# Performance work log

Hardware: AMD Instinct MI355X
Metric: run time of the kernel (lower is better)

Reference implementation:

```python
import jax, jax.numpy as jnp
import numpy as np

N_USERS = 20000
N_ITEMS = 30000
N = N_USERS + N_ITEMS          # total nodes
D = 64                          # embedding_dim
EXTRA = 1152                    # 768 metadata + 384 review
E = 500000                      # full-graph edges
NC = 100                        # clusters
HEADS = 2                       # per-layer GATConv heads
CG_HEADS = 4                    # GlobalGATOverClusters hard-codes heads=4
L = 2                           # num_layers
ED = 2                          # edge_dim


def _gat(x, ei, ea, lin, a_src, a_dst, lin_e, a_edge, bias, heads, nnodes):
    """PyG GATConv: add self loops (edge_attr fill='mean'), concat=False -> head mean."""
    C = a_src.shape[-1]
    loop = jnp.arange(nnodes)
    src = jnp.concatenate([ei[0], loop])
    dst = jnp.concatenate([ei[1], loop])
    ea_full = jnp.concatenate([ea, jnp.broadcast_to(ea.mean(0), (nnodes, ea.shape[1]))], 0)
    xh = (x @ lin).reshape(nnodes, heads, C)            # [N,H,C]
    asrc = (xh * a_src).sum(-1)                         # [N,H]
    adst = (xh * a_dst).sum(-1)
    eh = (ea_full @ lin_e).reshape(-1, heads, C)        # [Etot,H,C]
    ae = (eh * a_edge).sum(-1)                          # [Etot,H]
    al = jax.nn.leaky_relu(asrc[src] + adst[dst] + ae, 0.2)
    amax = jax.ops.segment_max(al, dst, num_segments=nnodes)
    ex = jnp.exp(al - amax[dst])
    s = jax.ops.segment_sum(ex, dst, num_segments=nnodes)
    w = ex / (s[dst] + 1e-16)
    out = jax.ops.segment_sum(xh[src] * w[..., None], dst, num_segments=nnodes)
    return out.mean(1) + bias


def _graph_norm(x, weight, bias, mean_scale, eps=1e-5):
    mean = x.mean(0)
    out = x - mean_scale * mean
    var = (out * out).mean(0)
    return weight * out * jax.lax.rsqrt(var + eps) + bias


def _forward(product_extra_features, user_emb, item_emb, fus_w1, fus_b1, fus_w2, fus_b2,
             full_edge_attr, gcn_w, gcn_b,
             cg_lin, cg_att_src, cg_att_dst, cg_lin_edge, cg_att_edge, cg_bias, cluster_edge_attr,
             gat_lin, gat_att_src, gat_att_dst, gat_lin_edge, gat_att_edge, gat_bias,
             gn_weight, gn_bias, gn_mean_scale,
             full_edge_index, cluster_assignment, cluster_edge_index):
    # fusion MLP on item side (dropout is identity at inference)
    h = jnp.maximum(jnp.concatenate([item_emb, product_extra_features], -1) @ fus_w1 + fus_b1, 0.0)
    enriched_items = h @ fus_w2 + fus_b2
    X = jnp.concatenate([user_emb, enriched_items], 0)  # [N, D]

    # per-cluster GCN == one GCN over intra-cluster edges + self loops;
    # nodes in clusters with zero intra edges keep original features
    ei0, ei1 = full_edge_index[0], full_edge_index[1]
    intra = cluster_assignment[ei0] == cluster_assignment[ei1]
    loop = jnp.arange(N)
    row = jnp.concatenate([ei0, loop])
    col = jnp.concatenate([ei1, loop])
    ew = jnp.concatenate([intra.astype(X.dtype), jnp.ones((N,), X.dtype)])
    deg = jax.ops.segment_sum(ew, col, num_segments=N)
    dinv = jnp.where(deg > 0, jax.lax.rsqrt(deg), 0.0)
    norm = dinv[row] * ew * dinv[col]
    xw = X @ gcn_w
    gcn_out = jax.ops.segment_sum(xw[row] * norm[:, None], col, num_segments=N) + gcn_b
    cl_has_edge = jax.ops.segment_sum(intra.astype(jnp.int32), cluster_assignment[ei0], num_segments=NC) > 0
    Xc = jnp.where(cl_has_edge[cluster_assignment][:, None], gcn_out, X)

    # mean pool per cluster
    cnt = jax.ops.segment_sum(jnp.ones((N,), X.dtype), cluster_assignment, num_segments=NC)
    pooled = jax.ops.segment_sum(Xc, cluster_assignment, num_segments=NC) / jnp.maximum(cnt, 1.0)[:, None]

    # global GAT over clusters (inter-cluster multigraph, precomputed)
    cl_upd = _gat(pooled, cluster_edge_index, cluster_edge_attr,
                  cg_lin, cg_att_src, cg_att_dst, cg_lin_edge, cg_att_edge, cg_bias, CG_HEADS, NC)
    Xcomb = Xc + cl_upd[cluster_assignment]

    # full-graph GAT stack with GraphNorm + residual ELU (dropout identity)
    for i in range(L):
        Xin = Xcomb
        g = _gat(Xcomb, full_edge_index, full_edge_attr,
                 gat_lin[i], gat_att_src[i], gat_att_dst[i],
                 gat_lin_edge[i], gat_att_edge[i], gat_bias[i], HEADS, N)
        g = _graph_norm(g, gn_weight[i], gn_bias[i], gn_mean_scale[i])
        Xcomb = jax.nn.elu(g + Xin)

    return Xcomb[:N_USERS], Xcomb[N_USERS:]


def setup_inputs() -> dict:
    rng = np.random.default_rng(0)
    fei = rng.integers(0, N, size=(2, E)).astype(np.int32)
    ca = rng.integers(0, NC, size=(N,)).astype(np.int32)
    fea = rng.random((E, ED)).astype(np.float32)
    # build_cluster_graph: one cluster edge per inter-cluster full edge
    cu, cv = ca[fei[0]], ca[fei[1]]
    m = cu != cv
    cei = np.stack([cu[m], cv[m]]).astype(np.int32)
    cea = fea[m]

    key = jax.random.key(0)
    ks = jax.random.split(key, 24)
    nrm = lambda k, shp, s=0.05: jax.random.normal(k, shp, dtype=jnp.float32) * s
    return {
        'product_extra_features': jax.random.normal(ks[0], (N_ITEMS, EXTRA), dtype=jnp.float32),
        'user_emb': nrm(ks[1], (N_USERS, D), 1.0),
        'item_emb': nrm(ks[2], (N_ITEMS, D), 1.0),
        'fus_w1': nrm(ks[3], (D + EXTRA, 2 * D)),
        'fus_b1': jnp.zeros((2 * D,), jnp.float32),
        'fus_w2': nrm(ks[4], (2 * D, D)),
        'fus_b2': jnp.zeros((D,), jnp.float32),
        'full_edge_attr': jnp.asarray(fea),
        'gcn_w': nrm(ks[5], (D, D)),
        'gcn_b': jnp.zeros((D,), jnp.float32),
        'cg_lin': nrm(ks[6], (D, CG_HEADS * D)),
        'cg_att_src': nrm(ks[7], (CG_HEADS, D)),
        'cg_att_dst': nrm(ks[8], (CG_HEADS, D)),
        'cg_lin_edge': nrm(ks[9], (ED, CG_HEADS * D)),
        'cg_att_edge': nrm(ks[10], (CG_HEADS, D)),
        'cg_bias': jnp.zeros((D,), jnp.float32),
        'cluster_edge_attr': jnp.asarray(cea),
        'gat_lin': nrm(ks[11], (L, D, HEADS * D)),
        'gat_att_src': nrm(ks[12], (L, HEADS, D)),
        'gat_att_dst': nrm(ks[13], (L, HEADS, D)),
        'gat_lin_edge': nrm(ks[14], (L, ED, HEADS * D)),
        'gat_att_edge': nrm(ks[15], (L, HEADS, D)),
        'gat_bias': jnp.zeros((L, D), jnp.float32),
        'gn_weight': jnp.ones((L, D), jnp.float32),
        'gn_bias': jnp.zeros((L, D), jnp.float32),
        'gn_mean_scale': jnp.ones((L, D), jnp.float32),
        'full_edge_index': jnp.asarray(fei),
        'cluster_assignment': jnp.asarray(ca),
        'cluster_edge_index': jnp.asarray(cei),
    }


def reference(product_extra_features, user_emb, item_emb, fus_w1, fus_b1, fus_w2, fus_b2,
              full_edge_attr, gcn_w, gcn_b,
              cg_lin, cg_att_src, cg_att_dst, cg_lin_edge, cg_att_edge, cg_bias, cluster_edge_attr,
              gat_lin, gat_att_src, gat_att_dst, gat_lin_edge, gat_att_edge, gat_bias,
              gn_weight, gn_bias, gn_mean_scale,
              full_edge_index, cluster_assignment, cluster_edge_index):
    return _forward(product_extra_features, user_emb, item_emb, fus_w1, fus_b1, fus_w2, fus_b2,
                    full_edge_attr, gcn_w, gcn_b,
                    cg_lin, cg_att_src, cg_att_dst, cg_lin_edge, cg_att_edge, cg_bias, cluster_edge_attr,
                    gat_lin, gat_att_src, gat_att_dst, gat_lin_edge, gat_att_edge, gat_bias,
                    gn_weight, gn_bias, gn_mean_scale,
                    full_edge_index, cluster_assignment, cluster_edge_index)
```

## Files before the change

kernel.cpp:

```cpp
#include <hip/hip_runtime.h>
#include <hip/hip_bf16.h>

#define N_USERS 20000
#define N_ITEMS 30000
#define NTOT    50000
#define DIM     64
#define EXTRA_D 1152
#define E_EDGES 500000
#define NC      100
#define KTOT    1216
#define KSTEPS  38
#define PPART   16
#define SPART   128

#define B_FEI  1954
#define B_W1   608
#define B_W2   32
#define B_CEI  256
#define PREP_GRID (B_FEI+B_W1+B_W2+B_CEI)

#define FUS_BLKS ((N_ITEMS+127)/128)
#define SCAN1_BLKS ((NTOT+1023)/1024)
#define B_COPY 1250
#define B_CC   64
#define FUS_GRID (FUS_BLKS+SCAN1_BLKS+1+B_COPY+B_CC)

#define SC3_BLKS ((NTOT+255)/256)
#define FILL_BLKS ((E_EDGES+255)/256)
#define DEG_BLKS ((NTOT+3)/4)

typedef __attribute__((ext_vector_type(8))) short short8;
typedef __attribute__((ext_vector_type(4))) float v4f;

__device__ __forceinline__ float wred_sum(float v){
#pragma unroll
  for(int o=32;o;o>>=1) v += __shfl_xor(v,o,64);
  return v;
}
__device__ __forceinline__ int wred_sumi(int v){
#pragma unroll
  for(int o=32;o;o>>=1) v += __shfl_xor(v,o,64);
  return v;
}
__device__ __forceinline__ float lrelu(float x){ return x>0.f? x : 0.2f*x; }
__device__ __forceinline__ short f2bf(float f){
  unsigned u=__float_as_uint(f);
  unsigned r=(u + 0x7FFFu + ((u>>16)&1u))>>16;
  return (short)r;
}
__device__ __forceinline__ unsigned pack_bf2(float x, float y){
  return (unsigned)(unsigned short)f2bf(x) | ((unsigned)(unsigned short)f2bf(y)<<16);
}

__global__ __launch_bounds__(256) void prep_edges_kernel(
    const float* __restrict__ w1, short* __restrict__ w1t,
    const float* __restrict__ w2, short* __restrict__ w2t,
    const int* __restrict__ ca,
    const int* __restrict__ fei, const float* __restrict__ fea,
    int* __restrict__ cnt_dst, int* __restrict__ clflag, int* __restrict__ degI,
    float2* __restrict__ partA,
    const int* __restrict__ cei, const float* __restrict__ cea, int Ec,
    int* __restrict__ ccnt_dst, float2* __restrict__ partB)
{
  __shared__ int hist[NC];
  __shared__ float2 w4[4];
  const int b=blockIdx.x, t=threadIdx.x;
  const int lane=t&63, wv=t>>6;
  if(b < B_FEI){
    int e = b*256+t;
    float a0=0.f,a1=0.f;
    if(e<E_EDGES){
      int s=fei[e], d=fei[E_EDGES+e];
      atomicAdd(&cnt_dst[d],1);
      int cs=ca[s];
      if(cs==ca[d]){ clflag[cs]=1; atomicAdd(&degI[d],1); }
      float2 v=*(const float2*)(fea+2*e);
      a0=v.x; a1=v.y;
    }
    a0=wred_sum(a0); a1=wred_sum(a1);
    if(lane==0) w4[wv]=make_float2(a0,a1);
    __syncthreads();
    if(t==0){ float2 r=w4[0]; for(int i=1;i<4;i++){r.x+=w4[i].x; r.y+=w4[i].y;} partA[b]=r; }
  } else if(b < B_FEI+B_W1){
    int i = (b-B_FEI)*256+t;
    int row = i>>7, n = i&127;
    int s = row>>5, kk = row&31;
    w1t[s*4096 + n*32 + kk] = f2bf(w1[i]);
  } else if(b < B_FEI+B_W1+B_W2){
    int i = (b-B_FEI-B_W1)*256+t;
    int n = i>>6, c = i&63;
    w2t[c*128 + n] = f2bf(w2[i]);
  } else {
    int bb = b-(B_FEI+B_W1+B_W2);
    for(int i=t;i<NC;i+=256) hist[i]=0;
    __syncthreads();
    float a0=0.f,a1=0.f;
    for(int e=bb*256+t; e<Ec; e+=B_CEI*256){
      atomicAdd(&hist[cei[Ec+e]],1);
      float2 v=*(const float2*)(cea+2*e);
      a0+=v.x; a1+=v.y;
    }
    a0=wred_sum(a0); a1=wred_sum(a1);
    if(lane==0) w4[wv]=make_float2(a0,a1);
    __syncthreads();
// ... 233 lines not shown
    for(int i=t;i<4096;i+=256) Wl[i]=gw[i];
    __syncthreads();
    for(int r=bb*4+wv; r<NTOT; r+=1024*4){
      rowb[wv][lane]=X[(size_t)r*64+lane];
      float acc=0.f;
#pragma unroll 8
      for(int k=0;k<64;k++) acc+=rowb[wv][k]*Wl[k*64+lane];
      xw[(size_t)r*64+lane]=acc;
    }
  }
}

__global__ __launch_bounds__(256) void fill_kernel(
    const int* __restrict__ fei, const float* __restrict__ fea,
    int* __restrict__ fillptr, int2* __restrict__ slot2,
    const int* __restrict__ cei, const float* __restrict__ cea, int Ec,
    int* __restrict__ cfillp, int* __restrict__ cslot_src, float2* __restrict__ cslot_ea)
{
  __shared__ int hist[NC];
  __shared__ int base[NC];
  const int b=blockIdx.x, t=threadIdx.x;
  if(b<FILL_BLKS){
    int e=b*256+t;
    if(e<E_EDGES){
      int dst=fei[E_EDGES+e], src=fei[e];
      int pos=atomicAdd(&fillptr[dst],1);
      float2 v=*(const float2*)(fea+2*e);
      slot2[pos]=make_int2(src,(int)pack_bf2(v.x,v.y));
    }
  } else {
    int bb=b-FILL_BLKS;
    const int chunk=(Ec+127)/128;
    const int beg=bb*chunk;
    const int end=min(beg+chunk,Ec);
    for(int i=t;i<NC;i+=256) hist[i]=0;
    __syncthreads();
    for(int e=beg+t;e<end;e+=256) atomicAdd(&hist[cei[Ec+e]],1);
    __syncthreads();
    for(int i=t;i<NC;i+=256){
      int h=hist[i];
      base[i] = h ? atomicAdd(&cfillp[i],h) : 0;
      hist[i]=0;
    }
    __syncthreads();
    for(int e=beg+t;e<end;e+=256){
      int d=cei[Ec+e];
      int pos = base[d] + atomicAdd(&hist[d],1);
      cslot_src[pos]=cei[e];
      cslot_ea[pos]=make_float2(cea[2*e],cea[2*e+1]);
    }
  }
}

__global__ __launch_bounds__(256) void gcn_agg_kernel(const float* __restrict__ X,
    const float* __restrict__ xw, const float* __restrict__ gcn_b,
    const int* __restrict__ offs, const int2* __restrict__ slot2, const int* __restrict__ ca,
    const float* __restrict__ dinv, const int* __restrict__ flag,
    float* __restrict__ Xc, float* __restrict__ psum){
  __shared__ float2 stg[4][64];
  int lane=threadIdx.x&63, wv=threadIdx.x>>6;
  int n=blockIdx.x*4+wv;
  int beg=offs[n], end=offs[n+1], myca=ca[n];
  float acc=0.f;
  for(int c0=beg;c0<end;c0+=64){
    int j=c0+lane;
    float coef=0.f; int s=0;
    if(j<end){
      s=slot2[j].x;
      if(ca[s]==myca) coef=dinv[s];
    }
    stg[wv][lane]=make_float2(__int_as_float(s),coef);
    unsigned long long bal=__ballot(coef!=0.f);
    while(bal){
      int k=__builtin_ctzll(bal); bal&=bal-1;
      float2 sc=stg[wv][k];
      acc += sc.y * xw[(size_t)__float_as_int(sc.x)*64+lane];
    }
  }
  float gout = dinv[n]*acc + gcn_b[lane];
  float xc = flag[myca] ? gout : X[(size_t)n*64+lane];
  Xc[(size_t)n*64+lane]=xc;
  atomicAdd(&psum[(size_t)(blockIdx.x&(PPART-1))*NC*64 + myca*64+lane], xc);
}

__global__ __launch_bounds__(256) void cluster_prep_kernel(const float* __restrict__ psum,
    const int* __restrict__ ccnt, const float* __restrict__ cg_lin,
    const float* __restrict__ as_, const float* __restrict__ ad_,
    float* __restrict__ xh_c, float* __restrict__ asrc_c, float* __restrict__ adst_c){
  __shared__ float prow[64];
  const int c=blockIdx.x, t=threadIdx.x;
  if(t<64){
    float a=0.f;
#pragma unroll
    for(int p=0;p<PPART;p++) a += psum[(size_t)p*NC*64 + c*64 + t];
    prow[t]=a/fmaxf((float)ccnt[c],1.f);
  }
  __syncthreads();
  float acc=0.f;
#pragma unroll 8
  for(int k=0;k<64;k++) acc += prow[k]*cg_lin[k*256+t];
  xh_c[c*256+t]=acc;
  int lane=t&63, hh=t>>6;
  float s=wred_sum(acc*as_[hh*64+lane]);
  float d=wred_sum(acc*ad_[hh*64+lane]);
  if(lane==0){ asrc_c[c*4+hh]=s; adst_c[c*4+hh]=d; }
}
__global__ __launch_bounds__(256) void cluster_agg_kernel(
    const int* __restrict__ coffs, const int* __restrict__ cslot_src, const float2* __restrict__ cslot_ea,
    const float* __restrict__ asrc_c, const float* __restrict__ adst_c, const float* __restrict__ coefs,
    const float* __restrict__ xh_c, const float* __restrict__ cg_bias, float* __restrict__ cl_upd)
{
  __shared__ float sas[NC*4];
  __shared__ float sW[NC*4];
  __shared__ float ssum[4];
  __shared__ float red[4][64];
  const int c=blockIdx.x, t=threadIdx.x;
  for(int i=t;i<NC*4;i+=256){ sas[i]=asrc_c[i]; sW[i]=0.f; }
  __syncthreads();
  float ad[4], A0[4], A1[4];
#pragma unroll
  for(int h=0;h<4;h++){ ad[h]=adst_c[c*4+h]; A0[h]=coefs[8+h]; A1[h]=coefs[12+h]; }
  const int beg=coffs[c], end=coffs[c+1];
  for(int j=beg+t;j<end;j+=256){
    int s=cslot_src[j]; float2 e=cslot_ea[j];
#pragma unroll
    for(int h=0;h<4;h++){
      float al=lrelu(sas[s*4+h]+ad[h]+e.x*A0[h]+e.y*A1[h]);
      atomicAdd(&sW[s*4+h], __expf(al));
    }
  }
  if(t<4){
    float al=lrelu(sas[c*4+t]+ad[t]+coefs[6]*A0[t]+coefs[7]*A1[t]);
    atomicAdd(&sW[c*4+t], __expf(al));
  }
  __syncthreads();
  const int h=t>>6, lane=t&63;
  float p=0.f;
  if(lane<NC)    p += sW[lane*4+h];
  if(lane+64<NC) p += sW[(lane+64)*4+h];
  p=wred_sum(p);
  if(lane==0) ssum[h]=p+1e-16f;
  __syncthreads();
  float inv=1.f/ssum[h];
  float acc=0.f;
  for(int s=0;s<NC;s++) acc += sW[s*4+h]*xh_c[s*256+h*64+lane];
  red[h][lane]=acc*inv;
  __syncthreads();
  if(t<64) cl_upd[c*64+t]=0.25f*(red[0][t]+red[1][t]+red[2][t]+red[3][t])+cg_bias[t];
}

__global__ __launch_bounds__(256) void gat_xh0_kernel(const float* __restrict__ Xc,
    const float* __restrict__ cl_upd, const int* __restrict__ ca,
    const float* __restrict__ lin, const float* __restrict__ att_s, const float* __restrict__ att_d,
    float2* __restrict__ xh2, float* __restrict__ asrc, float* __restrict__ adst,
    float* __restrict__ Xa){
  __shared__ __align__(16) float Wl[64*128];
  __shared__ float rowb[4][64];
  int t=threadIdx.x;
  for(int i=t;i<8192;i+=256) Wl[i]=lin[i];
  __syncthreads();
  int lane=t&63, wv=t>>6;
  float as0=att_s[lane], as1=att_s[64+lane], ad0=att_d[lane], ad1=att_d[64+lane];
  for(int r=blockIdx.x*4+wv; r<NTOT; r+=gridDim.x*4){
    float xv = Xc[(size_t)r*64+lane] + cl_upd[ca[r]*64+lane];
    Xa[(size_t)r*64+lane]=xv;
    rowb[wv][lane]=xv;
    float x0=0.f,x1=0.f;
#pragma unroll 8
    for(int k=0;k<64;k++){ float q=rowb[wv][k]; x0+=q*Wl[k*128+lane]; x1+=q*Wl[k*128+64+lane]; }
    xh2[(size_t)r*64+lane]=make_float2(x0,x1);
    float p0=wred_sum(x0*as0);
    float p1=wred_sum(x1*as1);
    float q0=wred_sum(x0*ad0);
    float q1=wred_sum(x1*ad1);
    if(lane==0){ asrc[2*r]=p0; asrc[2*r+1]=p1; adst[2*r]=q0; adst[2*r+1]=q1; }
  }
}
__global__ __launch_bounds__(256) void gat_xh1_kernel(const float* __restrict__ g,
    const float* __restrict__ Xres, const float* __restrict__ spart,
    const float* __restrict__ gnw, const float* __restrict__ gnb, const float* __restrict__ gnms,
    const float* __restrict__ lin, const float* __restrict__ att_s, const float* __restrict__ att_d,
    float2* __restrict__ xh2, float* __restrict__ asrc, float* __restrict__ adst,
    float* __restrict__ Xb){
  __shared__ __align__(16) float Wl[64*128];
  __shared__ float rowb[4][64];
  __shared__ float sm[4][64], sv[4][64];
  int t=threadIdx.x;
  int lane=t&63, wv=t>>6;
  for(int i=t;i<8192;i+=256) Wl[i]=lin[i];
  {
    float a0=0.f,a1=0.f;
    for(int p=wv;p<SPART;p+=4){ a0+=spart[p*128+lane]; a1+=spart[p*128+64+lane]; }
    sm[wv][lane]=a0; sv[wv][lane]=a1;
  }
  __syncthreads();
  const float invN = 1.f/(float)NTOT;
  float m=(sm[0][lane]+sm[1][lane]+sm[2][lane]+sm[3][lane])*invN;
  float vsum=(sv[0][lane]+sv[1][lane]+sv[2][lane]+sv[3][lane])*invN;
  float mm=gnms[lane]*m;
  float gwv=rsqrtf(vsum - 2.f*mm*m + mm*mm + 1e-5f)*gnw[lane];
  float gbv=gnb[lane];
  float as0=att_s[lane], as1=att_s[64+lane], ad0=att_d[lane], ad1=att_d[64+lane];
  for(int r=blockIdx.x*4+wv; r<NTOT; r+=gridDim.x*4){
    float z=(g[(size_t)r*64+lane]-mm)*gwv+gbv + Xres[(size_t)r*64+lane];
    float xv = z>0.f? z : __expf(z)-1.f;
    Xb[(size_t)r*64+lane]=xv;
    rowb[wv][lane]=xv;
    float x0=0.f,x1=0.f;
#pragma unroll 8
    for(int k=0;k<64;k++){ float q=rowb[wv][k]; x0+=q*Wl[k*128+lane]; x1+=q*Wl[k*128+64+lane]; }
    xh2[(size_t)r*64+lane]=make_float2(x0,x1);
    float p0=wred_sum(x0*as0);
    float p1=wred_sum(x1*as1);
    float q0=wred_sum(x0*ad0);
    float q1=wred_sum(x1*ad1);
    if(lane==0){ asrc[2*r]=p0; asrc[2*r+1]=p1; adst[2*r]=q0; adst[2*r+1]=q1; }
  }
}

__global__ __launch_bounds__(256) void gat_agg_kernel(const float2* __restrict__ xh2,
    const float2* __restrict__ asrc, const float2* __restrict__ adst,
    const int* __restrict__ offs, const int2* __restrict__ slot2,
    const float* __restrict__ coefs, int layer, const float* __restrict__ bias,
    float* __restrict__ g, float* __restrict__ spart){
  __shared__ float4 stg[4][64];
  __shared__ float s1[64], s2[64];
  int t=threadIdx.x;
  int lane=t&63, wv=t>>6;
  if(t<64){ s1[t]=0.f; s2[t]=0.f; }
  __syncthreads();
  int n=blockIdx.x*4+wv;
  float A00=coefs[16+layer*2+0], A01=coefs[16+layer*2+1];
  float A10=coefs[20+layer*2+0], A11=coefs[20+layer*2+1];
  int beg=offs[n], end=offs[n+1];
  float2 adn=adst[n];
  float s0=0.f,sB=0.f,acc0=0.f,acc1=0.f;
  for(int c0=beg;c0<end;c0+=64){
    int j=c0+lane;
    float ex0=0.f,ex1=0.f; int s=0;
    if(j<end){
      int2 sl=slot2[j];
      s=sl.x;
      unsigned p=(unsigned)sl.y;
      float e0=__uint_as_float(p<<16);
      float e1=__uint_as_float(p&0xffff0000u);
      float2 a=asrc[s];
      ex0=__expf(lrelu(a.x+adn.x+e0*A00+e1*A10));
      ex1=__expf(lrelu(a.y+adn.y+e0*A01+e1*A11));
    }
    s0+=ex0; sB+=ex1;
    stg[wv][lane]=make_float4(__int_as_float(s),ex0,ex1,0.f);
    int cnt=min(64,end-c0);
    int k=0;
    for(; k+4<=cnt; k+=4){
      float4 w0=stg[wv][k], w1=stg[wv][k+1], w2=stg[wv][k+2], w3=stg[wv][k+3];
      float2 x0=xh2[(size_t)__float_as_int(w0.x)*64+lane];
      float2 x1=xh2[(size_t)__float_as_int(w1.x)*64+lane];
      float2 x2=xh2[(size_t)__float_as_int(w2.x)*64+lane];
      float2 x3=xh2[(size_t)__float_as_int(w3.x)*64+lane];
      acc0 += w0.y*x0.x + w1.y*x1.x + w2.y*x2.x + w3.y*x3.x;
      acc1 += w0.z*x0.y + w1.z*x1.y + w2.z*x2.y + w3.z*x3.y;
    }
    for(; k<cnt; k++){
      float4 ws=stg[wv][k];
      float2 xv=xh2[(size_t)__float_as_int(ws.x)*64+lane];
      acc0 += ws.y*xv.x;
      acc1 += ws.z*xv.y;
    }
  }
  s0=wred_sum(s0); sB=wred_sum(sB);
  float gv = 0.5f*(acc0/(s0+1e-16f)+acc1/(sB+1e-16f))+bias[lane];
  g[(size_t)n*64+lane]=gv;
  atomicAdd(&s1[lane],gv);
  atomicAdd(&s2[lane],gv*gv);
  __syncthreads();
  float* dstp = spart + (size_t)(blockIdx.x&(SPART-1))*128;
  if(t<64) atomicAdd(&dstp[t],s1[t]);
  else if(t<128) atomicAdd(&dstp[t],s2[t-64]);
}

__global__ __launch_bounds__(256) void gnorm_elu_kernel(const float* __restrict__ g,
    const float* __restrict__ Xin, const float* __restrict__ spart,
    const float* __restrict__ gw, const float* __restrict__ gb, const float* __restrict__ gms,
    float* __restrict__ outp){
  __shared__ float sst[2][128];
  const float invN = 1.f/(float)NTOT;
  int t=threadIdx.x;
  {
    int d=t&127, hf=t>>7;
    float a=0.f;
    for(int p=hf*64;p<hf*64+64;p++) a+=spart[p*128+d];
    sst[hf][d]=a;
  }
  __syncthreads();
  int i0=blockIdx.x*256+t;
  int d0=(i0&15)*4;
  float mmv[4],gwv[4],gbv[4];
#pragma unroll
  for(int j=0;j<4;j++){
    int d=d0+j;
    float m=(sst[0][d]+sst[1][d])*invN;
    float mm=gms[d]*m;
    mmv[j]=mm;
    gwv[j]=rsqrtf((sst[0][64+d]+sst[1][64+d])*invN-2.f*mm*m+mm*mm+1e-5f)*gw[d];
    gbv[j]=gb[d];
  }
  for(int i=i0;i<NTOT*16;i+=gridDim.x*256){
    float4 gv=((const float4*)g)[i];
    float4 xv=((const float4*)Xin)[i];
    float4 o; float z;
    z=(gv.x-mmv[0])*gwv[0]+gbv[0]+xv.x; o.x = z>0.f? z : __expf(z)-1.f;
    z=(gv.y-mmv[1])*gwv[1]+gbv[1]+xv.y; o.y = z>0.f? z : __expf(z)-1.f;
    z=(gv.z-mmv[2])*gwv[2]+gbv[2]+xv.z; o.z = z>0.f? z : __expf(z)-1.f;
    z=(gv.w-mmv[3])*gwv[3]+gbv[3]+xv.w; o.w = z>0.f? z : __expf(z)-1.f;
    ((float4*)outp)[i]=o;
  }
}

extern "C" void kernel_launch(void* const* d_in, const int* in_sizes, int n_in,
                              void* d_out, int out_size, void* d_ws, size_t ws_size,
                              hipStream_t stream)
{
  const float* extra = (const float*)d_in[0];
  const float* user  = (const float*)d_in[1];
  const float* item  = (const float*)d_in[2];
  const float* fw1 = (const float*)d_in[3];
  const float* fb1 = (const float*)d_in[4];
  const float* fw2 = (const float*)d_in[5];
  const float* fb2 = (const float*)d_in[6];
  const float* fea = (const float*)d_in[7];
  const float* gcn_w = (const float*)d_in[8];
  const float* gcn_b = (const float*)d_in[9];
  const float* cg_lin = (const float*)d_in[10];
  const float* cg_as = (const float*)d_in[11];
  const float* cg_ad = (const float*)d_in[12];
  const float* cg_le = (const float*)d_in[13];
  const float* cg_ae = (const float*)d_in[14];
  const float* cg_bias = (const float*)d_in[15];
  const float* cea = (const float*)d_in[16];
  const float* gat_lin = (const float*)d_in[17];
  const float* gat_as = (const float*)d_in[18];
  const float* gat_ad = (const float*)d_in[19];
  const float* gat_le = (const float*)d_in[20];
  const float* gat_ae = (const float*)d_in[21];
  const float* gat_bias = (const float*)d_in[22];
  const float* gn_w = (const float*)d_in[23];
  const float* gn_b = (const float*)d_in[24];
  const float* gn_ms = (const float*)d_in[25];
  const int* fei = (const int*)d_in[26];
  const int* ca  = (const int*)d_in[27];
  const int* cei = (const int*)d_in[28];
  const int Ec = in_sizes[16]/2;
  float* outp = (float*)d_out;

  char* w = (char*)d_ws;
  auto alloc=[&](size_t b)->char*{ char* p=w; w += (b+255)&~(size_t)255; return p; };

  char* z0 = w;
  int* cnt_dst = (int*)alloc((size_t)NTOT*4);
  int* degI = (int*)alloc((size_t)NTOT*4);
  int* clflag = (int*)alloc(NC*4);
  int* ccnt = (int*)alloc(NC*4);
  int* ccnt_dst = (int*)alloc(NC*4);
  float* psum = (float*)alloc((size_t)PPART*NC*64*4);
  float* spart0 = (float*)alloc((size_t)SPART*128*4);
  float* spart1 = (float*)alloc((size_t)SPART*128*4);
  size_t zbytes = (size_t)(w - z0);

  float2* partA = (float2*)alloc(2048*8);
  float2* partB = (float2*)alloc(256*8);
  float* coefs = (float*)alloc(32*4);
  int* offs = (int*)alloc((size_t)(NTOT+1)*4);
  int* incl = (int*)alloc((size_t)NTOT*4);
  int* bsum = (int*)alloc(64*4);
  int* fillptr = (int*)alloc((size_t)NTOT*4);
  int2* slot2 = (int2*)alloc((size_t)(E_EDGES+NTOT)*8);
  int* coffs = (int*)alloc((size_t)(NC+1)*4);
  int* cfillp = (int*)alloc((size_t)NC*4);
  int* cslot_src = (int*)alloc((size_t)E_EDGES*4);
  float2* cslot_ea = (float2*)alloc((size_t)E_EDGES*8);
  float* dinv = (float*)alloc((size_t)NTOT*4);
  float* xh_c = (float*)alloc(NC*256*4);
  float* asrc_c = (float*)alloc(NC*4*4);
  float* adst_c = (float*)alloc(NC*4*4);
  float* cl_upd = (float*)alloc(NC*64*4);
  float* asrc = (float*)alloc((size_t)NTOT*2*4);
  float* adst = (float*)alloc((size_t)NTOT*2*4);
  short* w1t = (short*)alloc((size_t)KSTEPS*4096*2);
  short* w2t = (short*)alloc((size_t)64*128*2);
  float* bufA = (float*)alloc((size_t)NTOT*64*4);
  float* bufB = (float*)alloc((size_t)NTOT*64*4);
  float* bufC = (float*)alloc((size_t)NTOT*64*4);
  float* bufD = (float*)alloc((size_t)NTOT*64*4);
  float* bufE = (float*)alloc((size_t)NTOT*128*4);

  float* X  = bufA; float* g  = bufA;
  float* Xc = bufB;
  float* xw = bufC; float* Xb = bufC;
  float* Xa = bufD;
  float2* xh2 = (float2*)bufE;

  hipMemsetAsync(z0, 0, zbytes, stream);

  prep_edges_kernel<<<PREP_GRID,256,0,stream>>>(fw1, w1t, fw2, w2t, ca,
                                              fei, fea, cnt_dst, clflag, degI, partA,
                                              cei, cea, Ec, ccnt_dst, partB);
  fus_scan_kernel<<<FUS_GRID,256,0,stream>>>(item, extra, w1t, fb1, w2t, fb2, X,
                                              partA, partB, Ec, cg_le, cg_ae, gat_le, gat_ae, coefs,
                                              cnt_dst, incl, bsum, user, ca, ccnt);
  mid_kernel<<<SC3_BLKS+1+1024,256,0,stream>>>(incl, cnt_dst, bsum, offs, fillptr, coefs, slot2,
                                              degI, dinv, ccnt_dst, coffs, cfillp,
                                              X, gcn_w, xw);
  fill_kernel<<<FILL_BLKS+128,256,0,stream>>>(fei, fea, fillptr, slot2,
                                              cei, cea, Ec, cfillp, cslot_src, cslot_ea);

  gcn_agg_kernel<<<DEG_BLKS,256,0,stream>>>(X, xw, gcn_b, offs, slot2, ca, dinv, clflag, Xc, psum);
  cluster_prep_kernel<<<NC,256,0,stream>>>(psum, ccnt, cg_lin, cg_as, cg_ad, xh_c, asrc_c, adst_c);
  cluster_agg_kernel<<<NC,256,0,stream>>>(coffs, cslot_src, cslot_ea, asrc_c, adst_c, coefs,
                                          xh_c, cg_bias, cl_upd);

  gat_xh0_kernel<<<1024,256,0,stream>>>(Xc, cl_upd, ca, gat_lin, gat_as, gat_ad,
                                        xh2, asrc, adst, Xa);
  gat_agg_kernel<<<DEG_BLKS,256,0,stream>>>(xh2, (const float2*)asrc, (const float2*)adst,
                                            offs, slot2, coefs, 0, gat_bias, g, spart0);
  gat_xh1_kernel<<<1024,256,0,stream>>>(g, Xa, spart0, gn_w, gn_b, gn_ms,
                                        gat_lin+64*128, gat_as+128, gat_ad+128,
                                        xh2, asrc, adst, Xb);
  gat_agg_kernel<<<DEG_BLKS,256,0,stream>>>(xh2, (const float2*)asrc, (const float2*)adst,
                                            offs, slot2, coefs, 1, gat_bias+64, g, spart1);
  gnorm_elu_kernel<<<512,256,0,stream>>>(g, Xb, spart1, gn_w+64, gn_b+64, gn_ms+64, outp);
}
```

Measured before the change: 690.2 us.

## Fuse post-fill GCN/cluster/GAT/norm kernels into one persistent kernel with grid barriers

Replaces the eight tail kernel launches with a single persistent kernel of 1024 blocks. It runs GCN aggregation, cluster prep, cluster attention, two GAT transform and aggregation layers, and the final GraphNorm+ELU as grid-stride stages. The stages are separated by a software grid barrier that uses per-block flags and a release counter. It also reuses activation buffers through aliasing, which removes one full N×64 buffer. The goal is to cut launch gaps and inter-kernel drain; the cost is that blocks sit idle during the cluster-only stages, plus barrier latency. Correctness depends on all 1024 blocks being co-resident, with a timeout guard.

```diff
diff --git a/kernel.cpp b/kernel.cpp
--- a/kernel.cpp
+++ b/kernel.cpp
@@ -27,7 +27,9 @@
 
 #define SC3_BLKS ((NTOT+255)/256)
 #define FILL_BLKS ((E_EDGES+255)/256)
-#define DEG_BLKS ((NTOT+3)/4)
+
+#define GRID_C 1024
+#define NSTRIDE (GRID_C*4)
 
 typedef __attribute__((ext_vector_type(8))) short short8;
 typedef __attribute__((ext_vector_type(4))) float v4f;
@@ -50,6 +52,38 @@
 }
 __device__ __forceinline__ unsigned pack_bf2(float x, float y){
   return (unsigned)(unsigned short)f2bf(x) | ((unsigned)(unsigned short)f2bf(y)<<16);
+}
+
+__device__ __forceinline__ void grid_bar(int* __restrict__ flags, int* __restrict__ rel, int gen){
+  __syncthreads();
+  const int t=threadIdx.x;
+  if(t==0){
+    __threadfence();
+    __hip_atomic_store(&flags[blockIdx.x], gen, __ATOMIC_RELEASE, __HIP_MEMORY_SCOPE_AGENT);
+  }
+  if(blockIdx.x==0){
+    long guard=0;
+    for(;;){
+      int ok=1;
+#pragma unroll
+      for(int i=0;i<GRID_C/256;i++){
+        if(__hip_atomic_load(&flags[t+i*256], __ATOMIC_ACQUIRE, __HIP_MEMORY_SCOPE_AGENT) < gen) ok=0;
+      }
+      if(__syncthreads_and(ok)) break;
+      if(++guard > 200000000L) break;
+      __builtin_amdgcn_s_sleep(16);
+    }
+    if(t==0) __hip_atomic_store(rel, gen, __ATOMIC_RELEASE, __HIP_MEMORY_SCOPE_AGENT);
+  } else {
+    if(t==0){
+      long guard=0;
+      while(__hip_atomic_load(rel, __ATOMIC_ACQUIRE, __HIP_MEMORY_SCOPE_AGENT) < gen){
+        __builtin_amdgcn_s_sleep(16);
+        if(++guard > 200000000L) break;
+      }
+    }
+    __syncthreads();
+  }
 }
 
 __global__ __launch_bounds__(256) void prep_edges_kernel(
@@ -389,268 +423,307 @@
   }
 }
 
-__global__ __launch_bounds__(256) void gcn_agg_kernel(const float* __restrict__ X,
-    const float* __restrict__ xw, const float* __restrict__ gcn_b,
+__global__ __launch_bounds__(256,4) void tail_persist_kernel(
+    const float* __restrict__ X, const float* __restrict__ xw, const float* __restrict__ gcn_b,
     const int* __restrict__ offs, const int2* __restrict__ slot2, const int* __restrict__ ca,
-    const float* __restrict__ dinv, const int* __restrict__ flag,
-    float* __restrict__ Xc, float* __restrict__ psum){
-  __shared__ float2 stg[4][64];
-  int lane=threadIdx.x&63, wv=threadIdx.x>>6;
-  int n=blockIdx.x*4+wv;
-  int beg=offs[n], end=offs[n+1], myca=ca[n];
-  float acc=0.f;
-  for(int c0=beg;c0<end;c0+=64){
-    int j=c0+lane;
-    float coef=0.f; int s=0;
-    if(j<end){
-      s=slot2[j].x;
-      if(ca[s]==myca) coef=dinv[s];
-    }
-    stg[wv][lane]=make_float2(__int_as_float(s),coef);
-    unsigned long long bal=__ballot(coef!=0.f);
-    while(bal){
-      int k=__builtin_ctzll(bal); bal&=bal-1;
-      float2 sc=stg[wv][k];
-      acc += sc.y * xw[(size_t)__float_as_int(sc.x)*64+lane];
-    }
-  }
-  float gout = dinv[n]*acc + gcn_b[lane];
-  float xc = flag[myca] ? gout : X[(size_t)n*64+lane];
-  Xc[(size_t)n*64+lane]=xc;
-  atomicAdd(&psum[(size_t)(blockIdx.x&(PPART-1))*NC*64 + myca*64+lane], xc);
-}
-
-__global__ __launch_bounds__(256) void cluster_prep_kernel(const float* __restrict__ psum,
+    const float* __restrict__ dinv, const int* __restrict__ flag, float* __restrict__ psum,
     const int* __restrict__ ccnt, const float* __restrict__ cg_lin,
-    const float* __restrict__ as_, const float* __restrict__ ad_,
-    float* __restrict__ xh_c, float* __restrict__ asrc_c, float* __restrict__ adst_c){
-  __shared__ float prow[64];
-  const int c=blockIdx.x, t=threadIdx.x;
-  if(t<64){
-    float a=0.f;
-#pragma unroll
-    for(int p=0;p<PPART;p++) a += psum[(size_t)p*NC*64 + c*64 + t];
-    prow[t]=a/fmaxf((float)ccnt[c],1.f);
-  }
-  __syncthreads();
-  float acc=0.f;
+    const float* __restrict__ cg_as, const float* __restrict__ cg_ad,
+    const int* __restrict__ coffs, const int* __restrict__ cslot_src, const float2* __restrict__ cslot_ea,
+    const float* __restrict__ coefs, const float* __restrict__ cg_bias,
+    float* __restrict__ xh_c, float* __restrict__ asrc_c, float* __restrict__ adst_c,
+    float* __restrict__ cl_upd,
+    const float* __restrict__ gat_lin, const float* __restrict__ gat_as, const float* __restrict__ gat_ad,
+    const float* __restrict__ gat_bias,
+    const float* __restrict__ gn_w, const float* __restrict__ gn_b, const float* __restrict__ gn_ms,
+    float* __restrict__ Xc, float* __restrict__ Xa, float* __restrict__ Xb, float* __restrict__ g,
+    float2* __restrict__ xh2, float* __restrict__ asrc, float* __restrict__ adst,
+    float* __restrict__ spart0, float* __restrict__ spart1,
+    int* __restrict__ bflags, int* __restrict__ brel, float* __restrict__ outp)
+{
+  __shared__ __align__(16) char smraw[35840];
+  const int t=threadIdx.x, lane=t&63, wv=t>>6;
+  const int wbase = blockIdx.x*4+wv;
+  const float invN = 1.f/(float)NTOT;
+
+  {
+    float2 (*stg)[64] = (float2(*)[64])smraw;
+    for(int n=wbase; n<NTOT; n+=NSTRIDE){
+      int beg=offs[n], end=offs[n+1], myca=ca[n];
+      float acc=0.f;
+      for(int c0=beg;c0<end;c0+=64){
+        int j=c0+lane;
+        float coef=0.f; int s=0;
+        if(j<end){ s=slot2[j].x; if(ca[s]==myca) coef=dinv[s]; }
+        stg[wv][lane]=make_float2(__int_as_float(s),coef);
+        unsigned long long bal=__ballot(coef!=0.f);
+        while(bal){
+          int k=__builtin_ctzll(bal); bal&=bal-1;
+          float2 sc=stg[wv][k];
+          acc += sc.y * xw[(size_t)__float_as_int(sc.x)*64+lane];
+        }
+      }
+      float gout = dinv[n]*acc + gcn_b[lane];
+      float xc = flag[myca] ? gout : X[(size_t)n*64+lane];
+      Xc[(size_t)n*64+lane]=xc;
+      atomicAdd(&psum[(size_t)(blockIdx.x&(PPART-1))*NC*64 + myca*64+lane], xc);
+    }
+  }
+  grid_bar(bflags, brel, 1);
+
+  if(blockIdx.x < NC){
+    float* prow = (float*)smraw;
+    const int c=blockIdx.x;
+    if(t<64){
+      float a=0.f;
+#pragma unroll
+      for(int p=0;p<PPART;p++) a += psum[(size_t)p*NC*64 + c*64 + t];
+      prow[t]=a/fmaxf((float)ccnt[c],1.f);
+    }
+    __syncthreads();
+    float acc=0.f;
 #pragma unroll 8
-  for(int k=0;k<64;k++) acc += prow[k]*cg_lin[k*256+t];
-  xh_c[c*256+t]=acc;
-  int lane=t&63, hh=t>>6;
-  float s=wred_sum(acc*as_[hh*64+lane]);
-  float d=wred_sum(acc*ad_[hh*64+lane]);
-  if(lane==0){ asrc_c[c*4+hh]=s; adst_c[c*4+hh]=d; }
-}
-__global__ __launch_bounds__(256) void cluster_agg_kernel(
-    const int* __restrict__ coffs, const int* __restrict__ cslot_src, const float2* __restrict__ cslot_ea,
-    const float* __restrict__ asrc_c, const float* __restrict__ adst_c, const float* __restrict__ coefs,
-    const float* __restrict__ xh_c, const float* __restrict__ cg_bias, float* __restrict__ cl_upd)
-{
-  __shared__ float sas[NC*4];
-  __shared__ float sW[NC*4];
-  __shared__ float ssum[4];
-  __shared__ float red[4][64];
-  const int c=blockIdx.x, t=threadIdx.x;
-  for(int i=t;i<NC*4;i+=256){ sas[i]=asrc_c[i]; sW[i]=0.f; }
-  __syncthreads();
-  float ad[4], A0[4], A1[4];
-#pragma unroll
-  for(int h=0;h<4;h++){ ad[h]=adst_c[c*4+h]; A0[h]=coefs[8+h]; A1[h]=coefs[12+h]; }
-  const int beg=coffs[c], end=coffs[c+1];
-  for(int j=beg+t;j<end;j+=256){
-    int s=cslot_src[j]; float2 e=cslot_ea[j];
-#pragma unroll
-    for(int h=0;h<4;h++){
-      float al=lrelu(sas[s*4+h]+ad[h]+e.x*A0[h]+e.y*A1[h]);
-      atomicAdd(&sW[s*4+h], __expf(al));
-    }
-  }
-  if(t<4){
-    float al=lrelu(sas[c*4+t]+ad[t]+coefs[6]*A0[t]+coefs[7]*A1[t]);
-    atomicAdd(&sW[c*4+t], __expf(al));
-  }
-  __syncthreads();
-  const int h=t>>6, lane=t&63;
-  float p=0.f;
-  if(lane<NC)    p += sW[lane*4+h];
-  if(lane+64<NC) p += sW[(lane+64)*4+h];
-  p=wred_sum(p);
-  if(lane==0) ssum[h]=p+1e-16f;
-  __syncthreads();
-  float inv=1.f/ssum[h];
-  float acc=0.f;
-  for(int s=0;s<NC;s++) acc += sW[s*4+h]*xh_c[s*256+h*64+lane];
-  red[h][lane]=acc*inv;
-  __syncthreads();
-  if(t<64) cl_upd[c*64+t]=0.25f*(red[0][t]+red[1][t]+red[2][t]+red[3][t])+cg_bias[t];
-}
-
-__global__ __launch_bounds__(256) void gat_xh0_kernel(const float* __restrict__ Xc,
-    const float* __restrict__ cl_upd, const int* __restrict__ ca,
-    const float* __restrict__ lin, const float* __restrict__ att_s, const float* __restrict__ att_d,
-    float2* __restrict__ xh2, float* __restrict__ asrc, float* __restrict__ adst,
-    float* __restrict__ Xa){
-  __shared__ __align__(16) float Wl[64*128];
-  __shared__ float rowb[4][64];
-  int t=threadIdx.x;
-  for(int i=t;i<8192;i+=256) Wl[i]=lin[i];
-  __syncthreads();
-  int lane=t&63, wv=t>>6;
-  float as0=att_s[lane], as1=att_s[64+lane], ad0=att_d[lane], ad1=att_d[64+lane];
-  for(int r=blockIdx.x*4+wv; r<NTOT; r+=gridDim.x*4){
-    float xv = Xc[(size_t)r*64+lane] + cl_upd[ca[r]*64+lane];
-    Xa[(size_t)r*64+lane]=xv;
-    rowb[wv][lane]=xv;
-    float x0=0.f,x1=0.f;
+    for(int k=0;k<64;k++) acc += prow[k]*cg_lin[k*256+t];
+    xh_c[c*256+t]=acc;
+    float s=wred_sum(acc*cg_as[wv*64+lane]);
+    float d=wred_sum(acc*cg_ad[wv*64+lane]);
+    if(lane==0){ asrc_c[c*4+wv]=s; adst_c[c*4+wv]=d; }
+  }
+  grid_bar(bflags, brel, 2);
+
+  if(blockIdx.x < NC){
+    float* sas = (float*)smraw;
+    float* sW  = sas+400;
+    float* ssum= sW+400;
+    float* red = ssum+4;
+    const int c=blockIdx.x;
+    for(int i=t;i<NC*4;i+=256){ sas[i]=asrc_c[i]; sW[i]=0.f; }
+    __syncthreads();
+    float ad4[4], A0[4], A1[4];
+#pragma unroll
+    for(int h=0;h<4;h++){ ad4[h]=adst_c[c*4+h]; A0[h]=coefs[8+h]; A1[h]=coefs[12+h]; }
+    const int beg=coffs[c], end=coffs[c+1];
+    for(int j=beg+t;j<end;j+=256){
+      int s=cslot_src[j]; float2 e=cslot_ea[j];
+#pragma unroll
+      for(int h=0;h<4;h++){
+        float al=lrelu(sas[s*4+h]+ad4[h]+e.x*A0[h]+e.y*A1[h]);
+        atomicAdd(&sW[s*4+h], __expf(al));
+      }
+    }
+    if(t<4){
+      float al=lrelu(sas[c*4+t]+ad4[t]+coefs[6]*A0[t]+coefs[7]*A1[t]);
+      atomicAdd(&sW[c*4+t], __expf(al));
+    }
+    __syncthreads();
+    {
+      float p=0.f;
+      if(lane<NC)    p += sW[lane*4+wv];
+      if(lane+64<NC) p += sW[(lane+64)*4+wv];
+      p=wred_sum(p);
+      if(lane==0) ssum[wv]=p+1e-16f;
+    }
+    __syncthreads();
+    float inv=1.f/ssum[wv];
+    float acc=0.f;
+    for(int s=0;s<NC;s++) acc += sW[s*4+wv]*xh_c[s*256+wv*64+lane];
+    red[wv*64+lane]=acc*inv;
+    __syncthreads();
+    if(t<64) cl_upd[c*64+t]=0.25f*(red[t]+red[64+t]+red[128+t]+red[192+t])+cg_bias[t];
+  }
+  grid_bar(bflags, brel, 3);
+
+  {
+    float* Wl = (float*)smraw;
+    float (*rowb)[64] = (float(*)[64])(smraw+32768);
+    for(int i=t;i<8192;i+=256) Wl[i]=gat_lin[i];
+    __syncthreads();
+    float as0=gat_as[lane], as1=gat_as[64+lane], ad0=gat_ad[lane], ad1=gat_ad[64+lane];
+    for(int r=wbase; r<NTOT; r+=NSTRIDE){
+      float xv = Xc[(size_t)r*64+lane] + cl_upd[ca[r]*64+lane];
+      Xa[(size_t)r*64+lane]=xv;
+      rowb[wv][lane]=xv;
+      float x0=0.f,x1=0.f;
 #pragma unroll 8
-    for(int k=0;k<64;k++){ float q=rowb[wv][k]; x0+=q*Wl[k*128+lane]; x1+=q*Wl[k*128+64+lane]; }
-    xh2[(size_t)r*64+lane]=make_float2(x0,x1);
-    float p0=wred_sum(x0*as0);
-    float p1=wred_sum(x1*as1);
-    float q0=wred_sum(x0*ad0);
-    float q1=wred_sum(x1*ad1);
-    if(lane==0){ asrc[2*r]=p0; asrc[2*r+1]=p1; adst[2*r]=q0; adst[2*r+1]=q1; }
-  }
-}
-__global__ __launch_bounds__(256) void gat_xh1_kernel(const float* __restrict__ g,
-    const float* __restrict__ Xres, const float* __restrict__ spart,
-    const float* __restrict__ gnw, const float* __restrict__ gnb, const float* __restrict__ gnms,
-    const float* __restrict__ lin, const float* __restrict__ att_s, const float* __restrict__ att_d,
-    float2* __restrict__ xh2, float* __restrict__ asrc, float* __restrict__ adst,
-    float* __restrict__ Xb){
-  __shared__ __align__(16) float Wl[64*128];
-  __shared__ float rowb[4][64];
-  __shared__ float sm[4][64], sv[4][64];
-  int t=threadIdx.x;
-  int lane=t&63, wv=t>>6;
-  for(int i=t;i<8192;i+=256) Wl[i]=lin[i];
+      for(int k=0;k<64;k++){ float q=rowb[wv][k]; x0+=q*Wl[k*128+lane]; x1+=q*Wl[k*128+64+lane]; }
+      xh2[(size_t)r*64+lane]=make_float2(x0,x1);
+      float p0=wred_sum(x0*as0);
+      float p1=wred_sum(x1*as1);
+      float q0=wred_sum(x0*ad0);
+      float q1=wred_sum(x1*ad1);
+      if(lane==0){ asrc[2*r]=p0; asrc[2*r+1]=p1; adst[2*r]=q0; adst[2*r+1]=q1; }
+    }
+  }
+  grid_bar(bflags, brel, 4);
+
   {
-    float a0=0.f,a1=0.f;
-    for(int p=wv;p<SPART;p+=4){ a0+=spart[p*128+lane]; a1+=spart[p*128+64+lane]; }
-    sm[wv][lane]=a0; sv[wv][lane]=a1;
-  }
-  __syncthreads();
-  const float invN = 1.f/(float)NTOT;
-  float m=(sm[0][lane]+sm[1][lane]+sm[2][lane]+sm[3][lane])*invN;
-  float vsum=(sv[0][lane]+sv[1][lane]+sv[2][lane]+sv[3][lane])*invN;
-  float mm=gnms[lane]*m;
-  float gwv=rsqrtf(vsum - 2.f*mm*m + mm*mm + 1e-5f)*gnw[lane];
-  float gbv=gnb[lane];
-  float as0=att_s[lane], as1=att_s[64+lane], ad0=att_d[lane], ad1=att_d[64+lane];
-  for(int r=blockIdx.x*4+wv; r<NTOT; r+=gridDim.x*4){
-    float z=(g[(size_t)r*64+lane]-mm)*gwv+gbv + Xres[(size_t)r*64+lane];
-    float xv = z>0.f? z : __expf(z)-1.f;
-    Xb[(size_t)r*64+lane]=xv;
-    rowb[wv][lane]=xv;
-    float x0=0.f,x1=0.f;
+    float4 (*stg)[64] = (float4(*)[64])smraw;
+    float* s1 = (float*)(smraw+4096);
+    float* s2 = s1+64;
+    if(t<64){ s1[t]=0.f; s2[t]=0.f; }
+    __syncthreads();
+    float A00=coefs[16], A01=coefs[17], A10=coefs[20], A11=coefs[21];
+    for(int n=wbase; n<NTOT; n+=NSTRIDE){
+      int beg=offs[n], end=offs[n+1];
+      float2 adn=*(const float2*)(adst+2*n);
+      float s0=0.f,sB=0.f,acc0=0.f,acc1=0.f;
+      for(int c0=beg;c0<end;c0+=64){
+        int j=c0+lane;
+        float ex0=0.f,ex1=0.f; int s=0;
+        if(j<end){
+          int2 sl=slot2[j];
+          s=sl.x;
+          unsigned p=(unsigned)sl.y;
+          float e0=__uint_as_float(p<<16);
+          float e1=__uint_as_float(p&0xffff0000u);
+          float2 a=*(const float2*)(asrc+2*s);
+          ex0=__expf(lrelu(a.x+adn.x+e0*A00+e1*A10));
+          ex1=__expf(lrelu(a.y+adn.y+e0*A01+e1*A11));
+        }
+        s0+=ex0; sB+=ex1;
+        stg[wv][lane]=make_float4(__int_as_float(s),ex0,ex1,0.f);
+        int cnt=min(64,end-c0);
+        int k=0;
+        for(; k+4<=cnt; k+=4){
+          float4 w0=stg[wv][k], w1=stg[wv][k+1], w2=stg[wv][k+2], w3=stg[wv][k+3];
+          float2 x0=xh2[(size_t)__float_as_int(w0.x)*64+lane];
+          float2 x1=xh2[(size_t)__float_as_int(w1.x)*64+lane];
+          float2 x2=xh2[(size_t)__float_as_int(w2.x)*64+lane];
+          float2 x3=xh2[(size_t)__float_as_int(w3.x)*64+lane];
+          acc0 += w0.y*x0.x + w1.y*x1.x + w2.y*x2.x + w3.y*x3.x;
+          acc1 += w0.z*x0.y + w1.z*x1.y + w2.z*x2.y + w3.z*x3.y;
+        }
+        for(; k<cnt; k++){
+          float4 ws=stg[wv][k];
+          float2 xv=xh2[(size_t)__float_as_int(ws.x)*64+lane];
+          acc0 += ws.y*xv.x;
+          acc1 += ws.z*xv.y;
+        }
+      }
+      s0=wred_sum(s0); sB=wred_sum(sB);
+      float gv = 0.5f*(acc0/(s0+1e-16f)+acc1/(sB+1e-16f))+gat_bias[lane];
+      g[(size_t)n*64+lane]=gv;
+      atomicAdd(&s1[lane],gv);
+      atomicAdd(&s2[lane],gv*gv);
+    }
+    __syncthreads();
+    float* dstp = spart0 + (size_t)(blockIdx.x&(SPART-1))*128;
+    if(t<64) atomicAdd(&dstp[t],s1[t]);
+    else if(t<128) atomicAdd(&dstp[t],s2[t-64]);
+  }
+  grid_bar(bflags, brel, 5);
+
+  {
+    float* Wl = (float*)smraw;
+    float (*rowb)[64] = (float(*)[64])(smraw+32768);
+    float* smm = (float*)(smraw+33792);
+    float* svv = (float*)(smraw+34816);
+    for(int i=t;i<8192;i+=256) Wl[i]=gat_lin[8192+i];
+    {
+      float a0=0.f,a1=0.f;
+      for(int p=wv;p<SPART;p+=4){ a0+=spart0[p*128+lane]; a1+=spart0[p*128+64+lane]; }
+      smm[wv*64+lane]=a0; svv[wv*64+lane]=a1;
+    }
+    __syncthreads();
+    float m=(smm[lane]+smm[64+lane]+smm[128+lane]+smm[192+lane])*invN;
+    float vs=(svv[lane]+svv[64+lane]+svv[128+lane]+svv[192+lane])*invN;
+    float mm=gn_ms[lane]*m;
+    float gwv=rsqrtf(vs - 2.f*mm*m + mm*mm + 1e-5f)*gn_w[lane];
+    float gbv=gn_b[lane];
+    float as0=gat_as[128+lane], as1=gat_as[192+lane], ad0=gat_ad[128+lane], ad1=gat_ad[192+lane];
+    for(int r=wbase; r<NTOT; r+=NSTRIDE){
+      float z=(g[(size_t)r*64+lane]-mm)*gwv+gbv + Xa[(size_t)r*64+lane];
+      float xv = z>0.f? z : __expf(z)-1.f;
+      Xb[(size_t)r*64+lane]=xv;
+      rowb[wv][lane]=xv;
+      float x0=0.f,x1=0.f;
 #pragma unroll 8
-    for(int k=0;k<64;k++){ float q=rowb[wv][k]; x0+=q*Wl[k*128+lane]; x1+=q*Wl[k*128+64+lane]; }
-    xh2[(size_t)r*64+lane]=make_float2(x0,x1);
-    float p0=wred_sum(x0*as0);
-    float p1=wred_sum(x1*as1);
-    float q0=wred_sum(x0*ad0);
-    float q1=wred_sum(x1*ad1);
-    if(lane==0){ asrc[2*r]=p0; asrc[2*r+1]=p1; adst[2*r]=q0; adst[2*r+1]=q1; }
-  }
-}
-
-__global__ __launch_bounds__(256) void gat_agg_kernel(const float2* __restrict__ xh2,
-    const float2* __restrict__ asrc, const float2* __restrict__ adst,
-    const int* __restrict__ offs, const int2* __restrict__ slot2,
-    const float* __restrict__ coefs, int layer, const float* __restrict__ bias,
-    float* __restrict__ g, float* __restrict__ spart){
-  __shared__ float4 stg[4][64];
-  __shared__ float s1[64], s2[64];
-  int t=threadIdx.x;
-  int lane=t&63, wv=t>>6;
-  if(t<64){ s1[t]=0.f; s2[t]=0.f; }
-  __syncthreads();
-  int n=blockIdx.x*4+wv;
-  float A00=coefs[16+layer*2+0], A01=coefs[16+layer*2+1];
-  float A10=coefs[20+layer*2+0], A11=coefs[20+layer*2+1];
-  int beg=offs[n], end=offs[n+1];
-  float2 adn=adst[n];
-  float s0=0.f,sB=0.f,acc0=0.f,acc1=0.f;
-  for(int c0=beg;c0<end;c0+=64){
-    int j=c0+lane;
-    float ex0=0.f,ex1=0.f; int s=0;
-    if(j<end){
-      int2 sl=slot2[j];
-      s=sl.x;
-      unsigned p=(unsigned)sl.y;
-      float e0=__uint_as_float(p<<16);
-      float e1=__uint_as_float(p&0xffff0000u);
-      float2 a=asrc[s];
-      ex0=__expf(lrelu(a.x+adn.x+e0*A00+e1*A10));
-      ex1=__expf(lrelu(a.y+adn.y+e0*A01+e1*A11));
-    }
-    s0+=ex0; sB+=ex1;
-    stg[wv][lane]=make_float4(__int_as_float(s),ex0,ex1,0.f);
-    int cnt=min(64,end-c0);
-    int k=0;
-    for(; k+4<=cnt; k+=4){
-      float4 w0=stg[wv][k], w1=stg[wv][k+1], w2=stg[wv][k+2], w3=stg[wv][k+3];
-      float2 x0=xh2[(size_t)__float_as_int(w0.x)*64+lane];
-      float2 x1=xh2[(size_t)__float_as_int(w1.x)*64+lane];
-      float2 x2=xh2[(size_t)__float_as_int(w2.x)*64+lane];
-      float2 x3=xh2[(size_t)__float_as_int(w3.x)*64+lane];
-      acc0 += w0.y*x0.x + w1.y*x1.x + w2.y*x2.x + w3.y*x3.x;
-      acc1 += w0.z*x0.y + w1.z*x1.y + w2.z*x2.y + w3.z*x3.y;
-    }
-    for(; k<cnt; k++){
-      float4 ws=stg[wv][k];
-      float2 xv=xh2[(size_t)__float_as_int(ws.x)*64+lane];
-      acc0 += ws.y*xv.x;
-      acc1 += ws.z*xv.y;
-    }
-  }
-  s0=wred_sum(s0); sB=wred_sum(sB);
-  float gv = 0.5f*(acc0/(s0+1e-16f)+acc1/(sB+1e-16f))+bias[lane];
-  g[(size_t)n*64+lane]=gv;
-  atomicAdd(&s1[lane],gv);
-  atomicAdd(&s2[lane],gv*gv);
-  __syncthreads();
-  float* dstp = spart + (size_t)(blockIdx.x&(SPART-1))*128;
-  if(t<64) atomicAdd(&dstp[t],s1[t]);
-  else if(t<128) atomicAdd(&dstp[t],s2[t-64]);
-}
-
-__global__ __launch_bounds__(256) void gnorm_elu_kernel(const float* __restrict__ g,
-    const float* __restrict__ Xin, const float* __restrict__ spart,
-    const float* __restrict__ gw, const float* __restrict__ gb, const float* __restrict__ gms,
-    float* __restrict__ outp){
-  __shared__ float sst[2][128];
-  const float invN = 1.f/(float)NTOT;
-  int t=threadIdx.x;
+      for(int k=0;k<64;k++){ float q=rowb[wv][k]; x0+=q*Wl[k*128+lane]; x1+=q*Wl[k*128+64+lane]; }
+      xh2[(size_t)r*64+lane]=make_float2(x0,x1);
+      float p0=wred_sum(x0*as0);
+      float p1=wred_sum(x1*as1);
+      float q0=wred_sum(x0*ad0);
+      float q1=wred_sum(x1*ad1);
+      if(lane==0){ asrc[2*r]=p0; asrc[2*r+1]=p1; adst[2*r]=q0; adst[2*r+1]=q1; }
+    }
+  }
+  grid_bar(bflags, brel, 6);
+
   {
-    int d=t&127, hf=t>>7;
-    float a=0.f;
-    for(int p=hf*64;p<hf*64+64;p++) a+=spart[p*128+d];
-    sst[hf][d]=a;
-  }
-  __syncthreads();
-  int i0=blockIdx.x*256+t;
-  int d0=(i0&15)*4;
-  float mmv[4],gwv[4],gbv[4];
-#pragma unroll
-  for(int j=0;j<4;j++){
-    int d=d0+j;
-    float m=(sst[0][d]+sst[1][d])*invN;
-    float mm=gms[d]*m;
-    mmv[j]=mm;
-    gwv[j]=rsqrtf((sst[0][64+d]+sst[1][64+d])*invN-2.f*mm*m+mm*mm+1e-5f)*gw[d];
-    gbv[j]=gb[d];
-  }
-  for(int i=i0;i<NTOT*16;i+=gridDim.x*256){
-    float4 gv=((const float4*)g)[i];
-    float4 xv=((const float4*)Xin)[i];
-    float4 o; float z;
-    z=(gv.x-mmv[0])*gwv[0]+gbv[0]+xv.x; o.x = z>0.f? z : __expf(z)-1.f;
-    z=(gv.y-mmv[1])*gwv[1]+gbv[1]+xv.y; o.y = z>0.f? z : __expf(z)-1.f;
-    z=(gv.z-mmv[2])*gwv[2]+gbv[2]+xv.z; o.z = z>0.f? z : __expf(z)-1.f;
-    z=(gv.w-mmv[3])*gwv[3]+gbv[3]+xv.w; o.w = z>0.f? z : __expf(z)-1.f;
-    ((float4*)outp)[i]=o;
+    float4 (*stg)[64] = (float4(*)[64])smraw;
+    float* s1 = (float*)(smraw+4096);
+    float* s2 = s1+64;
+    if(t<64){ s1[t]=0.f; s2[t]=0.f; }
+    __syncthreads();
+    float A00=coefs[18], A01=coefs[19], A10=coefs[22], A11=coefs[23];
+    for(int n=wbase; n<NTOT; n+=NSTRIDE){
+      int beg=offs[n], end=offs[n+1];
+      float2 adn=*(const float2*)(adst+2*n);
+      float s0=0.f,sB=0.f,acc0=0.f,acc1=0.f;
+      for(int c0=beg;c0<end;c0+=64){
+        int j=c0+lane;
+        float ex0=0.f,ex1=0.f; int s=0;
+        if(j<end){
+          int2 sl=slot2[j];
+          s=sl.x;
+          unsigned p=(unsigned)sl.y;
+          float e0=__uint_as_float(p<<16);
+          float e1=__uint_as_float(p&0xffff0000u);
+          float2 a=*(const float2*)(asrc+2*s);
+          ex0=__expf(lrelu(a.x+adn.x+e0*A00+e1*A10));
+          ex1=__expf(lrelu(a.y+adn.y+e0*A01+e1*A11));
+        }
+        s0+=ex0; sB+=ex1;
+        stg[wv][lane]=make_float4(__int_as_float(s),ex0,ex1,0.f);
+        int cnt=min(64,end-c0);
+        int k=0;
+        for(; k+4<=cnt; k+=4){
+          float4 w0=stg[wv][k], w1=stg[wv][k+1], w2=stg[wv][k+2], w3=stg[wv][k+3];
+          float2 x0=xh2[(size_t)__float_as_int(w0.x)*64+lane];
+          float2 x1=xh2[(size_t)__float_as_int(w1.x)*64+lane];
+          float2 x2=xh2[(size_t)__float_as_int(w2.x)*64+lane];
+          float2 x3=xh2[(size_t)__float_as_int(w3.x)*64+lane];
+          acc0 += w0.y*x0.x + w1.y*x1.x + w2.y*x2.x + w3.y*x3.x;
+          acc1 += w0.z*x0.y + w1.z*x1.y + w2.z*x2.y + w3.z*x3.y;
+        }
+        for(; k<cnt; k++){
+          float4 ws=stg[wv][k];
+          float2 xv=xh2[(size_t)__float_as_int(ws.x)*64+lane];
+          acc0 += ws.y*xv.x;
+          acc1 += ws.z*xv.y;
+        }
+      }
+      s0=wred_sum(s0); sB=wred_sum(sB);
+      float gv = 0.5f*(acc0/(s0+1e-16f)+acc1/(sB+1e-16f))+gat_bias[64+lane];
+      g[(size_t)n*64+lane]=gv;
+      atomicAdd(&s1[lane],gv);
+      atomicAdd(&s2[lane],gv*gv);
+    }
+    __syncthreads();
+    float* dstp = spart1 + (size_t)(blockIdx.x&(SPART-1))*128;
+    if(t<64) atomicAdd(&dstp[t],s1[t]);
+    else if(t<128) atomicAdd(&dstp[t],s2[t-64]);
+  }
+  grid_bar(bflags, brel, 7);
+
+  {
+    float* sst = (float*)smraw;
+    {
+      int d=t&127, hf=t>>7;
+      float a=0.f;
+      for(int p=hf*64;p<hf*64+64;p++) a+=spart1[p*128+d];
+      sst[hf*128+d]=a;
+    }
+    __syncthreads();
+    float m=(sst[lane]+sst[128+lane])*invN;
+    float vs=(sst[64+lane]+sst[192+lane])*invN;
+    float mm=gn_ms[64+lane]*m;
+    float gwv=rsqrtf(vs - 2.f*mm*m + mm*mm + 1e-5f)*gn_w[64+lane];
+    float gbv=gn_b[64+lane];
+    for(int n=wbase; n<NTOT; n+=NSTRIDE){
+      float z=(g[(size_t)n*64+lane]-mm)*gwv+gbv + Xb[(size_t)n*64+lane];
+      outp[(size_t)n*64+lane] = z>0.f? z : __expf(z)-1.f;
+    }
   }
 }
 
@@ -702,6 +775,8 @@
   float* psum = (float*)alloc((size_t)PPART*NC*64*4);
   float* spart0 = (float*)alloc((size_t)SPART*128*4);
   float* spart1 = (float*)alloc((size_t)SPART*128*4);
+  int* bflags = (int*)alloc((size_t)GRID_C*4);
+  int* brel = (int*)alloc(256);
   size_t zbytes = (size_t)(w - z0);
 
   float2* partA = (float2*)alloc(2048*8);
@@ -728,13 +803,11 @@
   float* bufA = (float*)alloc((size_t)NTOT*64*4);
   float* bufB = (float*)alloc((size_t)NTOT*64*4);
   float* bufC = (float*)alloc((size_t)NTOT*64*4);
-  float* bufD = (float*)alloc((size_t)NTOT*64*4);
   float* bufE = (float*)alloc((size_t)NTOT*128*4);
 
   float* X  = bufA; float* g  = bufA;
-  float* Xc = bufB;
-  float* xw = bufC; float* Xb = bufC;
-  float* Xa = bufD;
+  float* Xc = bufB; float* Xb = bufB;
+  float* xw = bufC; float* Xa = bufC;
   float2* xh2 = (float2*)bufE;
 
   hipMemsetAsync(z0, 0, zbytes, stream);
@@ -751,19 +824,14 @@
   fill_kernel<<<FILL_BLKS+128,256,0,stream>>>(fei, fea, fillptr, slot2,
                                               cei, cea, Ec, cfillp, cslot_src, cslot_ea);
 
-  gcn_agg_kernel<<<DEG_BLKS,256,0,stream>>>(X, xw, gcn_b, offs, slot2, ca, dinv, clflag, Xc, psum);
-  cluster_prep_kernel<<<NC,256,0,stream>>>(psum, ccnt, cg_lin, cg_as, cg_ad, xh_c, asrc_c, adst_c);
-  cluster_agg_kernel<<<NC,256,0,stream>>>(coffs, cslot_src, cslot_ea, asrc_c, adst_c, coefs,
-                                          xh_c, cg_bias, cl_upd);
-
-  gat_xh0_kernel<<<1024,256,0,stream>>>(Xc, cl_upd, ca, gat_lin, gat_as, gat_ad,
-                                        xh2, asrc, adst, Xa);
-  gat_agg_kernel<<<DEG_BLKS,256,0,stream>>>(xh2, (const float2*)asrc, (const float2*)adst,
-                                            offs, slot2, coefs, 0, gat_bias, g, spart0);
-  gat_xh1_kernel<<<1024,256,0,stream>>>(g, Xa, spart0, gn_w, gn_b, gn_ms,
-                                        gat_lin+64*128, gat_as+128, gat_ad+128,
-                                        xh2, asrc, adst, Xb);
-  gat_agg_kernel<<<DEG_BLKS,256,0,stream>>>(xh2, (const float2*)asrc, (const float2*)adst,
-                                            offs, slot2, coefs, 1, gat_bias+64, g, spart1);
-  gnorm_elu_kernel<<<512,256,0,stream>>>(g, Xb, spart1, gn_w+64, gn_b+64, gn_ms+64, outp);
-}
+  tail_persist_kernel<<<GRID_C,256,0,stream>>>(X, xw, gcn_b,
+                                              offs, slot2, ca, dinv, clflag, psum,
+                                              ccnt, cg_lin, cg_as, cg_ad,
+                                              coffs, cslot_src, cslot_ea, coefs, cg_bias,
+                                              xh_c, asrc_c, adst_c, cl_upd,
+                                              gat_lin, gat_as, gat_ad, gat_bias,
+                                              gn_w, gn_b, gn_ms,
+                                              Xc, Xa, Xb, g,
+                                              xh2, asrc, adst, spart0, spart1,
+                                              bflags, brel, outp);
+}
```

New measurement: 2.049 ms. 197% more time.
